# Kernel tuning notes

Measured on AMD Instinct MI355X. Metric: run time of the kernel, lower is better.

## Reference

```python
import math
import jax, jax.numpy as jnp
import numpy as np

D_MODEL = 1024
HEADS = 16
B, S = 4, 2048


def setup_inputs() -> dict:
    key = jax.random.key(0)
    ks = jax.random.split(key, 8)
    scale = 1.0 / math.sqrt(D_MODEL)
    return {
        "q": jax.random.normal(ks[0], (B, S, D_MODEL), dtype=jnp.float32),
        "k": jax.random.normal(ks[1], (B, S, D_MODEL), dtype=jnp.float32),
        "v": jax.random.normal(ks[2], (B, S, D_MODEL), dtype=jnp.float32),
        "mask": jax.random.randint(ks[3], (B, S), 0, 2).astype(jnp.bool_),
        "alibi_mask": jax.random.normal(ks[4], (1, HEADS, S, S), dtype=jnp.float32),
        "Wq": jax.random.normal(ks[5], (D_MODEL, D_MODEL), dtype=jnp.float32) * scale,
        "Wk": jax.random.normal(ks[6], (D_MODEL, D_MODEL), dtype=jnp.float32) * scale,
        "Wv": jax.random.normal(ks[7], (D_MODEL, D_MODEL), dtype=jnp.float32) * scale,
    }


def _split_heads(x):
    b, s, d = x.shape
    return x.reshape(b, s, HEADS, d // HEADS).transpose(0, 2, 1, 3)  # [B,H,S,hd]


def reference(q, k, v, mask, alibi_mask, Wq, Wk, Wv):
    # QKV projections (Linear, no bias)
    qh = _split_heads(q @ Wq)
    kh = _split_heads(k @ Wk)
    vh = _split_heads(v @ Wv)
    depth = qh.shape[-1]
    # naive full attention matrix [B,H,Sq,Sk]
    w = jnp.einsum("bhqd,bhkd->bhqk", qh, kh) / math.sqrt(depth)
    # mask: [B,Sk] -> [B,1,1,Sk], True = masked
    w = jnp.where(mask[:, None, None, :], -jnp.inf, w)
    w = w + alibi_mask
    a = jax.nn.softmax(w, axis=-1)  # dropout p=0 -> identity
    out = jnp.einsum("bhqk,bhkd->bhqd", a, vh)
    # combine heads -> [B,S,D]
    out = out.transpose(0, 2, 1, 3).reshape(q.shape[0], q.shape[1], -1)
    return (out, a)
```

## Files before the change

### kernel.cpp

```cpp
#include <hip/hip_runtime.h>
#include <hip/hip_bf16.h>
#include <math.h>

constexpr int B  = 4;
constexpr int S  = 2048;
constexpr int D  = 1024;
constexpr int H  = 16;
constexpr int HD = 64;
constexpr float LOG2E  = 1.4426950408889634f;
constexpr float SCALE2 = 0.125f * LOG2E;

using f32x4 = __attribute__((ext_vector_type(4))) float;
using s16x8 = __attribute__((ext_vector_type(8))) short;
using u16x8 = __attribute__((ext_vector_type(8))) unsigned short;
using u16x4 = __attribute__((ext_vector_type(4))) unsigned short;

__device__ __forceinline__ unsigned short f2bf(float f) {
    union { float f; unsigned u; } x; x.f = f;
    unsigned r = x.u + 0x7fffu + ((x.u >> 16) & 1u);
    return (unsigned short)(r >> 16);
}
__device__ __forceinline__ unsigned short f2bf_fast(float f) {
    union { float f; unsigned u; } x; x.f = f;
    return (unsigned short)((x.u + 0x8000u) >> 16);
}
__device__ __forceinline__ float bf2f(unsigned short h) {
    union { unsigned u; float f; } x; x.u = ((unsigned)h) << 16;
    return x.f;
}
__device__ __forceinline__ float fexp2(float x) {
#if __has_builtin(__builtin_amdgcn_exp2f)
    return __builtin_amdgcn_exp2f(x);
#else
    return __expf(x * 0.6931471805599453f);
#endif
}

#define MFMA_BF16(Af, Bf, Cf) __builtin_amdgcn_mfma_f32_16x16x32_bf16(Af, Bf, Cf, 0, 0, 0)

__global__ __launch_bounds__(256) void k_wt3(const float* __restrict__ Wq,
                                             const float* __restrict__ Wk,
                                             const float* __restrict__ Wv,
                                             unsigned short* __restrict__ wqt,
                                             unsigned short* __restrict__ wkt,
                                             unsigned short* __restrict__ wvt) {
    const float* W = blockIdx.z == 0 ? Wq : (blockIdx.z == 1 ? Wk : Wv);
    unsigned short* Wt = blockIdx.z == 0 ? wqt : (blockIdx.z == 1 ? wkt : wvt);
    __shared__ unsigned short T[64][68];
    const int k0 = blockIdx.x * 64, n0 = blockIdx.y * 64;
    const int t = threadIdx.x;
    {
        const int kr = t >> 4, nc4 = (t & 15) * 4;
        for (int rr = 0; rr < 4; ++rr) {
            const int kk = kr + rr * 16;
            f32x4 wv = *reinterpret_cast<const f32x4*>(&W[(size_t)(k0 + kk) * D + n0 + nc4]);
#pragma unroll
            for (int j = 0; j < 4; ++j) T[nc4 + j][kk] = f2bf(wv[j]);
        }
    }
    __syncthreads();
    {
        const int nr = t >> 4, kc4 = (t & 15) * 4;
        for (int rr = 0; rr < 4; ++rr) {
            const int nn = nr + rr * 16;
            u16x4 o;
#pragma unroll
            for (int j = 0; j < 4; ++j) o[j] = T[nn][kc4 + j];
            *reinterpret_cast<u16x4*>(&Wt[(size_t)(n0 + nn) * D + k0 + kc4]) = o;
        }
    }
}

__global__ __launch_bounds__(256) void k_proj2(const float* __restrict__ Xq,
                                               const float* __restrict__ Xk,
                                               const unsigned short* __restrict__ wqt,
                                               const unsigned short* __restrict__ wkt,
                                               unsigned short* __restrict__ qh,
                                               unsigned short* __restrict__ kh) {
    const float* X = blockIdx.z == 0 ? Xq : Xk;
    const unsigned short* Wt = blockIdx.z == 0 ? wqt : wkt;
    unsigned short* Y = blockIdx.z == 0 ? qh : kh;

    __shared__ alignas(16) unsigned short As[128][72];
    __shared__ alignas(16) unsigned short Bs[128][72];
    const int bm = blockIdx.y * 128, bn = blockIdx.x * 128;
    const int t = threadIdx.x, w = t >> 6, l = t & 63;
    const int wr = w >> 1, wc = w & 1;
    const int lr = l & 15, lg = l >> 4;
    f32x4 acc[4][4] = {};

    for (int k0 = 0; k0 < D; k0 += 64) {
        {
            const int c4 = (t & 15) * 4;
            int row = t >> 4;
            for (int rr = 0; rr < 8; ++rr, row += 16) {
                f32x4 xv = *reinterpret_cast<const f32x4*>(&X[(size_t)(bm + row) * D + k0 + c4]);
                u16x4 hv;
#pragma unroll
                for (int j = 0; j < 4; ++j) hv[j] = f2bf(xv[j]);
                *reinterpret_cast<u16x4*>(&As[row][c4]) = hv;
            }
        }
        for (int i = 0; i < 4; ++i) {
            const int idx = t + i * 256;
            const int row = idx >> 3, c8 = (idx & 7) * 8;
            *reinterpret_cast<u16x8*>(&Bs[row][c8]) =
                *reinterpret_cast<const u16x8*>(&Wt[(size_t)(bn + row) * D + k0 + c8]);
        }
        __syncthreads();
#pragma unroll
        for (int kk = 0; kk < 2; ++kk) {
            s16x8 af[4], bf[4];
#pragma unroll
            for (int f = 0; f < 4; ++f) {
                af[f] = *reinterpret_cast<const s16x8*>(&As[wr * 64 + f * 16 + lr][kk * 32 + lg * 8]);
                bf[f] = *reinterpret_cast<const s16x8*>(&Bs[wc * 64 + f * 16 + lr][kk * 32 + lg * 8]);
            }
#pragma unroll
            for (int fm = 0; fm < 4; ++fm)
#pragma unroll
                for (int fn = 0; fn < 4; ++fn)
                    acc[fm][fn] = MFMA_BF16(af[fm], bf[fn], acc[fm][fn]);
        }
        __syncthreads();
    }
#pragma unroll
    for (int fm = 0; fm < 4; ++fm)
#pragma unroll
        for (int fn = 0; fn < 4; ++fn)
#pragma unroll
            for (int r = 0; r < 4; ++r) {
                const int m = bm + wr * 64 + fm * 16 + lg * 4 + r;
                const int n = bn + wc * 64 + fn * 16 + lr;
                const int b = m >> 11, s = m & (S - 1);
                const int h = n >> 6, e = n & 63;
                Y[(((size_t)(b * H + h) * S) + s) * HD + e] = f2bf(acc[fm][fn][r]);
            }
}

__global__ __launch_bounds__(256) void k_projv_mfma(const float* __restrict__ X,
                                                    const unsigned short* __restrict__ Wt,
                                                    unsigned short* __restrict__ VT) {
    __shared__ alignas(16) unsigned short SM[2][128][72];
    unsigned short (*As)[72] = SM[0];
    unsigned short (*Bs)[72] = SM[1];
    const int bm = blockIdx.y * 128, bn = blockIdx.x * 128;
    const int t = threadIdx.x, w = t >> 6, l = t & 63;
    const int wr = w >> 1, wc = w & 1;
    const int lr = l & 15, lg = l >> 4;
    f32x4 acc[4][4] = {};

    for (int k0 = 0; k0 < D; k0 += 64) {
        {
            const int c4 = (t & 15) * 4;
            int row = t >> 4;
            for (int rr = 0; rr < 8; ++rr, row += 16) {
                f32x4 xv = *reinterpret_cast<const f32x4*>(&X[(size_t)(bm + row) * D + k0 + c4]);
                u16x4 hv;
#pragma unroll
                for (int j = 0; j < 4; ++j) hv[j] = f2bf(xv[j]);
                *reinterpret_cast<u16x4*>(&As[row][c4]) = hv;
            }
        }
        for (int i = 0; i < 4; ++i) {
            const int idx = t + i * 256;
            const int row = idx >> 3, c8 = (idx & 7) * 8;
            *reinterpret_cast<u16x8*>(&Bs[row][c8]) =
                *reinterpret_cast<const u16x8*>(&Wt[(size_t)(bn + row) * D + k0 + c8]);
        }
        __syncthreads();
#pragma unroll
        for (int kk = 0; kk < 2; ++kk) {
            s16x8 af[4], bf[4];
#pragma unroll
            for (int f = 0; f < 4; ++f) {
                af[f] = *reinterpret_cast<const s16x8*>(&As[wr * 64 + f * 16 + lr][kk * 32 + lg * 8]);
                bf[f] = *reinterpret_cast<const s16x8*>(&Bs[wc * 64 + f * 16 + lr][kk * 32 + lg * 8]);
            }
#pragma unroll
            for (int fm = 0; fm < 4; ++fm)
#pragma unroll
                for (int fn = 0; fn < 4; ++fn)
                    acc[fm][fn] = MFMA_BF16(af[fm], bf[fn], acc[fm][fn]);
        }
        __syncthreads();
    }
    unsigned short (*T)[144] = reinterpret_cast<unsigned short(*)[144]>(&SM[0][0][0]);
#pragma unroll
    for (int fm = 0; fm < 4; ++fm)
#pragma unroll
        for (int fn = 0; fn < 4; ++fn)
#pragma unroll
            for (int r = 0; r < 4; ++r)
                T[wc * 64 + fn * 16 + lr][wr * 64 + fm * 16 + lg * 4 + r] = f2bf(acc[fm][fn][r]);
    __syncthreads();
    const int b = bm >> 11, s0 = bm & (S - 1);
    for (int it = 0; it < 8; ++it) {
        const int idx = t + it * 256;
        const int row = idx >> 4, c8 = (idx & 15) * 8;
        const int h = (bn + row) >> 6, e = (bn + row) & 63;
        *reinterpret_cast<u16x8*>(&VT[((size_t)(b * H + h) * HD + e) * S + s0 + c8]) =
            *reinterpret_cast<const u16x8*>(&T[row][c8]);
    }
}

__global__ __launch_bounds__(256) void k_abf16(const float* __restrict__ A,
                                               unsigned short* __restrict__ O) {
    const size_t N = (size_t)H * S * S;
    const size_t stride = (size_t)gridDim.x * 256 * 8;
    for (size_t i = ((size_t)blockIdx.x * 256 + threadIdx.x) * 8; i < N; i += stride) {
        f32x4 a0 = *reinterpret_cast<const f32x4*>(&A[i]);
        f32x4 a1 = *reinterpret_cast<const f32x4*>(&A[i + 4]);
        u16x8 o;
#pragma unroll
        for (int j = 0; j < 4; ++j) {
            o[j]     = f2bf(a0[j] * LOG2E);
            o[4 + j] = f2bf(a1[j] * LOG2E);
        }
        *reinterpret_cast<u16x8*>(&O[i]) = o;
    }
}

template <bool ABF16>
__global__ __launch_bounds__(512, 4) void k_sumexp(
    const unsigned short* __restrict__ QH, const unsigned short* __restrict__ KH,
    const float* __restrict__ ALIBI, const unsigned short* __restrict__ ABF,
    const int* __restrict__ MASK, float* __restrict__ INVL) {
    __shared__ alignas(16) unsigned short Ks[64][72];
    __shared__ alignas(16) unsigned short ALs[128][72];

    const int bid = blockIdx.x;
    const int wg = (bid & 7) * 128 + (bid >> 3);
    const int bh = wg >> 4, b = bh >> 4, h = bh & 15;
    const int q0 = (wg & 15) * 128;
    const int t = threadIdx.x, w = t >> 6, ln = t & 63;
    const int lr = ln & 15, lg = ln >> 4;
    const unsigned short NEGBIG = f2bf(-1e30f);
    const size_t hoff = (size_t)h * S * S;

    const unsigned short* Kb = KH + (size_t)bh * S * HD;

    s16x8 qf[2];
#pragma unroll
    for (int kk = 0; kk < 2; ++kk)
        qf[kk] = *reinterpret_cast<const s16x8*>(
            &QH[((size_t)bh * S + q0 + w * 16 + lr) * HD + kk * 32 + lg * 8]);

    float psum = 0.f;

    for (int k0 = 0; k0 < S; k0 += 64) {
        {
            const int row = t >> 3, c8 = (t & 7) * 8;
            *reinterpret_cast<u16x8*>(&Ks[row][c8]) =
                *reinterpret_cast<const u16x8*>(&Kb[(size_t)(k0 + row) * HD + c8]);
        }
#pragma unroll
        for (int i = 0; i < 2; ++i) {
            const int idx = t + i * 512, row = idx >> 3, c8 = (idx & 7) * 8;
            int4 m0 = *reinterpret_cast<const int4*>(&MASK[b * S + k0 + c8]);
            int4 m1 = *reinterpret_cast<const int4*>(&MASK[b * S + k0 + c8 + 4]);
            u16x8 av;
            if constexpr (ABF16) {
                av = *reinterpret_cast<const u16x8*>(&ABF[hoff + (size_t)(q0 + row) * S + k0 + c8]);
            } else {
                f32x4 a0 = *reinterpret_cast<const f32x4*>(&ALIBI[hoff + (size_t)(q0 + row) * S + k0 + c8]);
                f32x4 a1 = *reinterpret_cast<const f32x4*>(&ALIBI[hoff + (size_t)(q0 + row) * S + k0 + c8 + 4]);
#pragma unroll
                for (int j = 0; j < 4; ++j) {
                    av[j] = f2bf(a0[j] * LOG2E);
                    av[4 + j] = f2bf(a1[j] * LOG2E);
                }
            }
            u16x8 sv;
            sv[0] = m0.x ? NEGBIG : av[0];
            sv[1] = m0.y ? NEGBIG : av[1];
            sv[2] = m0.z ? NEGBIG : av[2];
            sv[3] = m0.w ? NEGBIG : av[3];
            sv[4] = m1.x ? NEGBIG : av[4];
            sv[5] = m1.y ? NEGBIG : av[5];
            sv[6] = m1.z ? NEGBIG : av[6];
            sv[7] = m1.w ? NEGBIG : av[7];
            *reinterpret_cast<u16x8*>(&ALs[row][c8]) = sv;
        }
        __syncthreads();

        f32x4 acc[4] = {};
#pragma unroll
        for (int kk = 0; kk < 2; ++kk)
#pragma unroll
            for (int fn = 0; fn < 4; ++fn) {
                s16x8 kf = *reinterpret_cast<const s16x8*>(&Ks[fn * 16 + lr][kk * 32 + lg * 8]);
                acc[fn] = MFMA_BF16(kf, qf[kk], acc[fn]);
            }
#pragma unroll
        for (int fn = 0; fn < 4; ++fn) {
            u16x4 alv = *reinterpret_cast<const u16x4*>(&ALs[w * 16 + lr][fn * 16 + lg * 4]);
            f32x4 al;
#pragma unroll
            for (int j = 0; j < 4; ++j) al[j] = bf2f(alv[j]);
            f32x4 sv = acc[fn] * SCALE2 + al;
            psum += fexp2(sv[0]) + fexp2(sv[1]) + fexp2(sv[2]) + fexp2(sv[3]);
        }
        __syncthreads();
    }

    psum += __shfl_xor(psum, 16, 64);
    psum += __shfl_xor(psum, 32, 64);
    if (lg == 0)
        INVL[(size_t)bh * S + q0 + w * 16 + lr] = 1.0f / psum;
}

template <bool ABF16>
__global__ __launch_bounds__(512, 4) void k_attn(
    const unsigned short* __restrict__ QH, const unsigned short* __restrict__ KH,
    const unsigned short* __restrict__ VT, const float* __restrict__ ALIBI,
    const unsigned short* __restrict__ ABF, const int* __restrict__ MASK,
    const float* __restrict__ INVL, float* __restrict__ Aout,
    float* __restrict__ OUT) {
    __shared__ alignas(16) unsigned short Ks[64][72];
    __shared__ alignas(16) unsigned short Vs[64][72];
    __shared__ alignas(16) unsigned short ALs[128][72];

    const int bid = blockIdx.x;
    const int wg = (bid & 7) * 128 + (bid >> 3);
    const int bh = wg >> 4, b = bh >> 4, h = bh & 15;
    const int q0 = (wg & 15) * 128;
    const int t = threadIdx.x, w = t >> 6, ln = t & 63;
    const int lr = ln & 15, lg = ln >> 4;
    const unsigned short NEGBIG = f2bf(-1e30f);
    const size_t hoff = (size_t)h * S * S;

    const unsigned short* Kb = KH + (size_t)bh * S * HD;
    const unsigned short* Vb = VT + (size_t)bh * HD * S;

    s16x8 qf[2];
#pragma unroll
    for (int kk = 0; kk < 2; ++kk)
        qf[kk] = *reinterpret_cast<const s16x8*>(
            &QH[((size_t)bh * S + q0 + w * 16 + lr) * HD + kk * 32 + lg * 8]);

    const float invl = INVL[(size_t)bh * S + q0 + w * 16 + lr];
    float* arow = Aout + ((size_t)bh * S + q0 + w * 16 + lr) * S;

    f32x4 oacc[4] = {};

    for (int k0 = 0; k0 < S; k0 += 64) {
        {
            const int row = t >> 3, c8 = (t & 7) * 8;
            *reinterpret_cast<u16x8*>(&Ks[row][c8]) =
                *reinterpret_cast<const u16x8*>(&Kb[(size_t)(k0 + row) * HD + c8]);
            *reinterpret_cast<u16x8*>(&Vs[row][c8]) =
                *reinterpret_cast<const u16x8*>(&Vb[(size_t)row * S + k0 + c8]);
        }
#pragma unroll
        for (int i = 0; i < 2; ++i) {
            const int idx = t + i * 512, row = idx >> 3, c8 = (idx & 7) * 8;
            int4 m0 = *reinterpret_cast<const int4*>(&MASK[b * S + k0 + c8]);
            int4 m1 = *reinterpret_cast<const int4*>(&MASK[b * S + k0 + c8 + 4]);
            u16x8 av;
            if constexpr (ABF16) {
                av = *reinterpret_cast<const u16x8*>(&ABF[hoff + (size_t)(q0 + row) * S + k0 + c8]);
            } else {
                f32x4 a0 = *reinterpret_cast<const f32x4*>(&ALIBI[hoff + (size_t)(q0 + row) * S + k0 + c8]);
                f32x4 a1 = *reinterpret_cast<const f32x4*>(&ALIBI[hoff + (size_t)(q0 + row) * S + k0 + c8 + 4]);
#pragma unroll
                for (int j = 0; j < 4; ++j) {
                    av[j] = f2bf(a0[j] * LOG2E);
                    av[4 + j] = f2bf(a1[j] * LOG2E);
                }
            }
            u16x8 sv;
            sv[0] = m0.x ? NEGBIG : av[0];
            sv[1] = m0.y ? NEGBIG : av[1];
            sv[2] = m0.z ? NEGBIG : av[2];
            sv[3] = m0.w ? NEGBIG : av[3];
            sv[4] = m1.x ? NEGBIG : av[4];
            sv[5] = m1.y ? NEGBIG : av[5];
            sv[6] = m1.z ? NEGBIG : av[6];
            sv[7] = m1.w ? NEGBIG : av[7];
            *reinterpret_cast<u16x8*>(&ALs[row][c8]) = sv;
        }
        __syncthreads();

        f32x4 acc[4] = {};
#pragma unroll
        for (int kk = 0; kk < 2; ++kk)
#pragma unroll
            for (int fn = 0; fn < 4; ++fn) {
                s16x8 kf = *reinterpret_cast<const s16x8*>(&Ks[fn * 16 + lr][kk * 32 + lg * 8]);
                acc[fn] = MFMA_BF16(kf, qf[kk], acc[fn]);
            }

#pragma unroll
        for (int fn = 0; fn < 4; ++fn) {
            u16x4 alv = *reinterpret_cast<const u16x4*>(&ALs[w * 16 + lr][fn * 16 + lg * 4]);
            f32x4 al;
#pragma unroll
            for (int j = 0; j < 4; ++j) al[j] = bf2f(alv[j]);
            f32x4 sv = acc[fn] * SCALE2 + al;
            f32x4 p;
#pragma unroll
            for (int j = 0; j < 4; ++j) p[j] = fexp2(sv[j]);
            p *= invl;
            __builtin_nontemporal_store(
                p, reinterpret_cast<f32x4*>(arow + k0 + fn * 16 + lg * 4));
            u16x4 pb;
#pragma unroll
            for (int j = 0; j < 4; ++j) pb[j] = f2bf_fast(p[j]);
            *reinterpret_cast<u16x4*>(&ALs[w * 16 + lr][fn * 16 + lg * 4]) = pb;
        }

#pragma unroll
        for (int c = 0; c < 2; ++c) {
            s16x8 pa = *reinterpret_cast<const s16x8*>(&ALs[w * 16 + lr][c * 32 + lg * 8]);
#pragma unroll
            for (int fn = 0; fn < 4; ++fn) {
                s16x8 vf = *reinterpret_cast<const s16x8*>(&Vs[fn * 16 + lr][c * 32 + lg * 8]);
                oacc[fn] = MFMA_BF16(pa, vf, oacc[fn]);
            }
        }
        __syncthreads();
    }

#pragma unroll
    for (int fn = 0; fn < 4; ++fn)
#pragma unroll
        for (int r = 0; r < 4; ++r)
            OUT[(size_t)(b * S + q0 + w * 16 + lg * 4 + r) * D + h * HD + fn * 16 + lr] =
                oacc[fn][r];
}

extern "C" void kernel_launch(void* const* d_in, const int* in_sizes, int n_in,
                              void* d_out, int out_size, void* d_ws, size_t ws_size,
                              hipStream_t stream) {
    const float* q     = (const float*)d_in[0];
    const float* k     = (const float*)d_in[1];
    const float* v     = (const float*)d_in[2];
    const int*   mask  = (const int*)d_in[3];
    const float* alibi = (const float*)d_in[4];
    const float* Wq    = (const float*)d_in[5];
    const float* Wk    = (const float*)d_in[6];
    const float* Wv    = (const float*)d_in[7];

    float* out = (float*)d_out;
    float* a   = out + (size_t)B * S * D;

    const size_t NH = (size_t)B * H * S * HD;
    unsigned short* qh  = (unsigned short*)d_ws;
    unsigned short* kh  = qh + NH;
    unsigned short* vT  = kh + NH;
    unsigned short* wqt = vT + NH;
    unsigned short* wkt = wqt + (size_t)D * D;
    unsigned short* wvt = wkt + (size_t)D * D;
    float*          invl = (float*)(wvt + (size_t)D * D);
    unsigned short* abf  = (unsigned short*)(invl + (size_t)B * H * S);

    const size_t need_bf16 =
        ((size_t)(abf - qh) + (size_t)H * S * S) * sizeof(unsigned short);
    const bool use_abf16 = ws_size >= need_bf16;

    const dim3 blk(256);

    k_wt3<<<dim3(D / 64, D / 64, 3), blk, 0, stream>>>(Wq, Wk, Wv, wqt, wkt, wvt);

    if (use_abf16)
        k_abf16<<<dim3(8192), blk, 0, stream>>>(alibi, abf);

    k_proj2<<<dim3(D / 128, (B * S) / 128, 2), blk, 0, stream>>>(q, k, wqt, wkt, qh, kh);
    k_projv_mfma<<<dim3(D / 128, (B * S) / 128), blk, 0, stream>>>(v, wvt, vT);

    if (use_abf16) {
        k_sumexp<true><<<dim3(1024), dim3(512), 0, stream>>>(
            qh, kh, alibi, abf, mask, invl);
        k_attn<true><<<dim3(1024), dim3(512), 0, stream>>>(
            qh, kh, vT, alibi, abf, mask, invl, a, out);
    } else {
        k_sumexp<false><<<dim3(1024), dim3(512), 0, stream>>>(
            qh, kh, alibi, abf, mask, invl);
        k_attn<false><<<dim3(1024), dim3(512), 0, stream>>>(
            qh, kh, vT, alibi, abf, mask, invl, a, out);
    }
}
```

Before: 665.3 us.

## Read fp32 alibi and mask directly in registers, drop bf16 pre-pass, double-buffer K/V

Removes the separate kernel that converted the alibi bias to bf16 and the shared-memory staging of bias+mask. Each lane now loads its fp32 alibi and mask values straight from global memory and folds them in with an fma. K/V tiles are double-buffered in shared memory so the next tile loads while the current one computes, and one barrier per iteration is removed. This cuts total alibi traffic and a launch, but relies on uncoalesced per-row global loads in the inner loop.

```diff
diff --git a/kernel.cpp b/kernel.cpp
--- a/kernel.cpp
+++ b/kernel.cpp
@@ -23,10 +23,6 @@
 __device__ __forceinline__ unsigned short f2bf_fast(float f) {
     union { float f; unsigned u; } x; x.f = f;
     return (unsigned short)((x.u + 0x8000u) >> 16);
-}
-__device__ __forceinline__ float bf2f(unsigned short h) {
-    union { unsigned u; float f; } x; x.u = ((unsigned)h) << 16;
-    return x.f;
 }
 __device__ __forceinline__ float fexp2(float x) {
 #if __has_builtin(__builtin_amdgcn_exp2f)
@@ -204,30 +200,11 @@
     }
 }
 
-__global__ __launch_bounds__(256) void k_abf16(const float* __restrict__ A,
-                                               unsigned short* __restrict__ O) {
-    const size_t N = (size_t)H * S * S;
-    const size_t stride = (size_t)gridDim.x * 256 * 8;
-    for (size_t i = ((size_t)blockIdx.x * 256 + threadIdx.x) * 8; i < N; i += stride) {
-        f32x4 a0 = *reinterpret_cast<const f32x4*>(&A[i]);
-        f32x4 a1 = *reinterpret_cast<const f32x4*>(&A[i + 4]);
-        u16x8 o;
-#pragma unroll
-        for (int j = 0; j < 4; ++j) {
-            o[j]     = f2bf(a0[j] * LOG2E);
-            o[4 + j] = f2bf(a1[j] * LOG2E);
-        }
-        *reinterpret_cast<u16x8*>(&O[i]) = o;
-    }
-}
-
-template <bool ABF16>
 __global__ __launch_bounds__(512, 4) void k_sumexp(
     const unsigned short* __restrict__ QH, const unsigned short* __restrict__ KH,
-    const float* __restrict__ ALIBI, const unsigned short* __restrict__ ABF,
-    const int* __restrict__ MASK, float* __restrict__ INVL) {
-    __shared__ alignas(16) unsigned short Ks[64][72];
-    __shared__ alignas(16) unsigned short ALs[128][72];
+    const float* __restrict__ ALIBI, const int* __restrict__ MASK,
+    float* __restrict__ INVL) {
+    __shared__ alignas(16) unsigned short Ks[2][64][72];
 
     const int bid = blockIdx.x;
     const int wg = (bid & 7) * 128 + (bid >> 3);
@@ -235,10 +212,10 @@
     const int q0 = (wg & 15) * 128;
     const int t = threadIdx.x, w = t >> 6, ln = t & 63;
     const int lr = ln & 15, lg = ln >> 4;
-    const unsigned short NEGBIG = f2bf(-1e30f);
-    const size_t hoff = (size_t)h * S * S;
 
     const unsigned short* Kb = KH + (size_t)bh * S * HD;
+    const float* alrow = ALIBI + ((size_t)h * S + q0 + w * 16 + lr) * S;
+    const int* mrow = MASK + b * S;
 
     s16x8 qf[2];
 #pragma unroll
@@ -246,62 +223,41 @@
         qf[kk] = *reinterpret_cast<const s16x8*>(
             &QH[((size_t)bh * S + q0 + w * 16 + lr) * HD + kk * 32 + lg * 8]);
 
+    auto stage_k = [&](int buf, int k0) {
+        const int row = t >> 3, c8 = (t & 7) * 8;
+        *reinterpret_cast<u16x8*>(&Ks[buf][row][c8]) =
+            *reinterpret_cast<const u16x8*>(&Kb[(size_t)(k0 + row) * HD + c8]);
+    };
+
     float psum = 0.f;
-
-    for (int k0 = 0; k0 < S; k0 += 64) {
-        {
-            const int row = t >> 3, c8 = (t & 7) * 8;
-            *reinterpret_cast<u16x8*>(&Ks[row][c8]) =
-                *reinterpret_cast<const u16x8*>(&Kb[(size_t)(k0 + row) * HD + c8]);
-        }
-#pragma unroll
-        for (int i = 0; i < 2; ++i) {
-            const int idx = t + i * 512, row = idx >> 3, c8 = (idx & 7) * 8;
-            int4 m0 = *reinterpret_cast<const int4*>(&MASK[b * S + k0 + c8]);
-            int4 m1 = *reinterpret_cast<const int4*>(&MASK[b * S + k0 + c8 + 4]);
-            u16x8 av;
-            if constexpr (ABF16) {
-                av = *reinterpret_cast<const u16x8*>(&ABF[hoff + (size_t)(q0 + row) * S + k0 + c8]);
-            } else {
-                f32x4 a0 = *reinterpret_cast<const f32x4*>(&ALIBI[hoff + (size_t)(q0 + row) * S + k0 + c8]);
-                f32x4 a1 = *reinterpret_cast<const f32x4*>(&ALIBI[hoff + (size_t)(q0 + row) * S + k0 + c8 + 4]);
-#pragma unroll
-                for (int j = 0; j < 4; ++j) {
-                    av[j] = f2bf(a0[j] * LOG2E);
-                    av[4 + j] = f2bf(a1[j] * LOG2E);
-                }
-            }
-            u16x8 sv;
-            sv[0] = m0.x ? NEGBIG : av[0];
-            sv[1] = m0.y ? NEGBIG : av[1];
-            sv[2] = m0.z ? NEGBIG : av[2];
-            sv[3] = m0.w ? NEGBIG : av[3];
-            sv[4] = m1.x ? NEGBIG : av[4];
-            sv[5] = m1.y ? NEGBIG : av[5];
-            sv[6] = m1.z ? NEGBIG : av[6];
-            sv[7] = m1.w ? NEGBIG : av[7];
-            *reinterpret_cast<u16x8*>(&ALs[row][c8]) = sv;
-        }
-        __syncthreads();
+    stage_k(0, 0);
+
+    for (int t16 = 0; t16 < 32; ++t16) {
+        const int cur = t16 & 1;
+        const int k0 = t16 * 64;
+        __syncthreads();
+        if (t16 < 31) stage_k(cur ^ 1, k0 + 64);
 
         f32x4 acc[4] = {};
 #pragma unroll
         for (int kk = 0; kk < 2; ++kk)
 #pragma unroll
             for (int fn = 0; fn < 4; ++fn) {
-                s16x8 kf = *reinterpret_cast<const s16x8*>(&Ks[fn * 16 + lr][kk * 32 + lg * 8]);
+                s16x8 kf = *reinterpret_cast<const s16x8*>(&Ks[cur][fn * 16 + lr][kk * 32 + lg * 8]);
                 acc[fn] = MFMA_BF16(kf, qf[kk], acc[fn]);
             }
 #pragma unroll
         for (int fn = 0; fn < 4; ++fn) {
-            u16x4 alv = *reinterpret_cast<const u16x4*>(&ALs[w * 16 + lr][fn * 16 + lg * 4]);
-            f32x4 al;
-#pragma unroll
-            for (int j = 0; j < 4; ++j) al[j] = bf2f(alv[j]);
-            f32x4 sv = acc[fn] * SCALE2 + al;
+            const int kc = k0 + fn * 16 + lg * 4;
+            f32x4 al = *reinterpret_cast<const f32x4*>(&alrow[kc]);
+            int4 mv = *reinterpret_cast<const int4*>(&mrow[kc]);
+            f32x4 sv;
+            sv[0] = mv.x ? -1e30f : fmaf(al[0], LOG2E, acc[fn][0] * SCALE2);
+            sv[1] = mv.y ? -1e30f : fmaf(al[1], LOG2E, acc[fn][1] * SCALE2);
+            sv[2] = mv.z ? -1e30f : fmaf(al[2], LOG2E, acc[fn][2] * SCALE2);
+            sv[3] = mv.w ? -1e30f : fmaf(al[3], LOG2E, acc[fn][3] * SCALE2);
             psum += fexp2(sv[0]) + fexp2(sv[1]) + fexp2(sv[2]) + fexp2(sv[3]);
         }
-        __syncthreads();
     }
 
     psum += __shfl_xor(psum, 16, 64);
@@ -310,16 +266,14 @@
         INVL[(size_t)bh * S + q0 + w * 16 + lr] = 1.0f / psum;
 }
 
-template <bool ABF16>
 __global__ __launch_bounds__(512, 4) void k_attn(
     const unsigned short* __restrict__ QH, const unsigned short* __restrict__ KH,
     const unsigned short* __restrict__ VT, const float* __restrict__ ALIBI,
-    const unsigned short* __restrict__ ABF, const int* __restrict__ MASK,
-    const float* __restrict__ INVL, float* __restrict__ Aout,
-    float* __restrict__ OUT) {
-    __shared__ alignas(16) unsigned short Ks[64][72];
-    __shared__ alignas(16) unsigned short Vs[64][72];
-    __shared__ alignas(16) unsigned short ALs[128][72];
+    const int* __restrict__ MASK, const float* __restrict__ INVL,
+    float* __restrict__ Aout, float* __restrict__ OUT) {
+    __shared__ alignas(16) unsigned short Ks[2][64][72];
+    __shared__ alignas(16) unsigned short Vs[2][64][72];
+    __shared__ alignas(16) unsigned short Ps[128][72];
 
     const int bid = blockIdx.x;
     const int wg = (bid & 7) * 128 + (bid >> 3);
@@ -327,11 +281,11 @@
     const int q0 = (wg & 15) * 128;
     const int t = threadIdx.x, w = t >> 6, ln = t & 63;
     const int lr = ln & 15, lg = ln >> 4;
-    const unsigned short NEGBIG = f2bf(-1e30f);
-    const size_t hoff = (size_t)h * S * S;
 
     const unsigned short* Kb = KH + (size_t)bh * S * HD;
     const unsigned short* Vb = VT + (size_t)bh * HD * S;
+    const float* alrow = ALIBI + ((size_t)h * S + q0 + w * 16 + lr) * S;
+    const int* mrow = MASK + b * S;
 
     s16x8 qf[2];
 #pragma unroll
@@ -342,84 +296,63 @@
     const float invl = INVL[(size_t)bh * S + q0 + w * 16 + lr];
     float* arow = Aout + ((size_t)bh * S + q0 + w * 16 + lr) * S;
 
+    auto stage_kv = [&](int buf, int k0) {
+        const int row = t >> 3, c8 = (t & 7) * 8;
+        *reinterpret_cast<u16x8*>(&Ks[buf][row][c8]) =
+            *reinterpret_cast<const u16x8*>(&Kb[(size_t)(k0 + row) * HD + c8]);
+        *reinterpret_cast<u16x8*>(&Vs[buf][row][c8]) =
+            *reinterpret_cast<const u16x8*>(&Vb[(size_t)row * S + k0 + c8]);
+    };
+
     f32x4 oacc[4] = {};
-
-    for (int k0 = 0; k0 < S; k0 += 64) {
-        {
-            const int row = t >> 3, c8 = (t & 7) * 8;
-            *reinterpret_cast<u16x8*>(&Ks[row][c8]) =
-                *reinterpret_cast<const u16x8*>(&Kb[(size_t)(k0 + row) * HD + c8]);
-            *reinterpret_cast<u16x8*>(&Vs[row][c8]) =
-                *reinterpret_cast<const u16x8*>(&Vb[(size_t)row * S + k0 + c8]);
-        }
-#pragma unroll
-        for (int i = 0; i < 2; ++i) {
-            const int idx = t + i * 512, row = idx >> 3, c8 = (idx & 7) * 8;
-            int4 m0 = *reinterpret_cast<const int4*>(&MASK[b * S + k0 + c8]);
-            int4 m1 = *reinterpret_cast<const int4*>(&MASK[b * S + k0 + c8 + 4]);
-            u16x8 av;
-            if constexpr (ABF16) {
-                av = *reinterpret_cast<const u16x8*>(&ABF[hoff + (size_t)(q0 + row) * S + k0 + c8]);
-            } else {
-                f32x4 a0 = *reinterpret_cast<const f32x4*>(&ALIBI[hoff + (size_t)(q0 + row) * S + k0 + c8]);
-                f32x4 a1 = *reinterpret_cast<const f32x4*>(&ALIBI[hoff + (size_t)(q0 + row) * S + k0 + c8 + 4]);
-#pragma unroll
-                for (int j = 0; j < 4; ++j) {
-                    av[j] = f2bf(a0[j] * LOG2E);
-                    av[4 + j] = f2bf(a1[j] * LOG2E);
-                }
-            }
-            u16x8 sv;
-            sv[0] = m0.x ? NEGBIG : av[0];
-            sv[1] = m0.y ? NEGBIG : av[1];
-            sv[2] = m0.z ? NEGBIG : av[2];
-            sv[3] = m0.w ? NEGBIG : av[3];
-            sv[4] = m1.x ? NEGBIG : av[4];
-            sv[5] = m1.y ? NEGBIG : av[5];
-            sv[6] = m1.z ? NEGBIG : av[6];
-            sv[7] = m1.w ? NEGBIG : av[7];
-            *reinterpret_cast<u16x8*>(&ALs[row][c8]) = sv;
-        }
-        __syncthreads();
+    stage_kv(0, 0);
+
+    for (int t16 = 0; t16 < 32; ++t16) {
+        const int cur = t16 & 1;
+        const int k0 = t16 * 64;
+        __syncthreads();
+        if (t16 < 31) stage_kv(cur ^ 1, k0 + 64);
 
         f32x4 acc[4] = {};
 #pragma unroll
         for (int kk = 0; kk < 2; ++kk)
 #pragma unroll
             for (int fn = 0; fn < 4; ++fn) {
-                s16x8 kf = *reinterpret_cast<const s16x8*>(&Ks[fn * 16 + lr][kk * 32 + lg * 8]);
+                s16x8 kf = *reinterpret_cast<const s16x8*>(&Ks[cur][fn * 16 + lr][kk * 32 + lg * 8]);
                 acc[fn] = MFMA_BF16(kf, qf[kk], acc[fn]);
             }
 
 #pragma unroll
         for (int fn = 0; fn < 4; ++fn) {
-            u16x4 alv = *reinterpret_cast<const u16x4*>(&ALs[w * 16 + lr][fn * 16 + lg * 4]);
-            f32x4 al;
-#pragma unroll
-            for (int j = 0; j < 4; ++j) al[j] = bf2f(alv[j]);
-            f32x4 sv = acc[fn] * SCALE2 + al;
+            const int kc = k0 + fn * 16 + lg * 4;
+            f32x4 al = *reinterpret_cast<const f32x4*>(&alrow[kc]);
+            int4 mv = *reinterpret_cast<const int4*>(&mrow[kc]);
+            f32x4 sv;
+            sv[0] = mv.x ? -1e30f : fmaf(al[0], LOG2E, acc[fn][0] * SCALE2);
+            sv[1] = mv.y ? -1e30f : fmaf(al[1], LOG2E, acc[fn][1] * SCALE2);
+            sv[2] = mv.z ? -1e30f : fmaf(al[2], LOG2E, acc[fn][2] * SCALE2);
+            sv[3] = mv.w ? -1e30f : fmaf(al[3], LOG2E, acc[fn][3] * SCALE2);
             f32x4 p;
 #pragma unroll
             for (int j = 0; j < 4; ++j) p[j] = fexp2(sv[j]);
             p *= invl;
             __builtin_nontemporal_store(
-                p, reinterpret_cast<f32x4*>(arow + k0 + fn * 16 + lg * 4));
+                p, reinterpret_cast<f32x4*>(arow + kc));
             u16x4 pb;
 #pragma unroll
             for (int j = 0; j < 4; ++j) pb[j] = f2bf_fast(p[j]);
-            *reinterpret_cast<u16x4*>(&ALs[w * 16 + lr][fn * 16 + lg * 4]) = pb;
+            *reinterpret_cast<u16x4*>(&Ps[w * 16 + lr][fn * 16 + lg * 4]) = pb;
         }
 
 #pragma unroll
         for (int c = 0; c < 2; ++c) {
-            s16x8 pa = *reinterpret_cast<const s16x8*>(&ALs[w * 16 + lr][c * 32 + lg * 8]);
+            s16x8 pa = *reinterpret_cast<const s16x8*>(&Ps[w * 16 + lr][c * 32 + lg * 8]);
 #pragma unroll
             for (int fn = 0; fn < 4; ++fn) {
-                s16x8 vf = *reinterpret_cast<const s16x8*>(&Vs[fn * 16 + lr][c * 32 + lg * 8]);
+                s16x8 vf = *reinterpret_cast<const s16x8*>(&Vs[cur][fn * 16 + lr][c * 32 + lg * 8]);
                 oacc[fn] = MFMA_BF16(pa, vf, oacc[fn]);
             }
         }
-        __syncthreads();
     }
 
 #pragma unroll
@@ -453,31 +386,14 @@
     unsigned short* wkt = wqt + (size_t)D * D;
     unsigned short* wvt = wkt + (size_t)D * D;
     float*          invl = (float*)(wvt + (size_t)D * D);
-    unsigned short* abf  = (unsigned short*)(invl + (size_t)B * H * S);
-
-    const size_t need_bf16 =
-        ((size_t)(abf - qh) + (size_t)H * S * S) * sizeof(unsigned short);
-    const bool use_abf16 = ws_size >= need_bf16;
 
     const dim3 blk(256);
 
     k_wt3<<<dim3(D / 64, D / 64, 3), blk, 0, stream>>>(Wq, Wk, Wv, wqt, wkt, wvt);
-
-    if (use_abf16)
-        k_abf16<<<dim3(8192), blk, 0, stream>>>(alibi, abf);
 
     k_proj2<<<dim3(D / 128, (B * S) / 128, 2), blk, 0, stream>>>(q, k, wqt, wkt, qh, kh);
     k_projv_mfma<<<dim3(D / 128, (B * S) / 128), blk, 0, stream>>>(v, wvt, vT);
 
-    if (use_abf16) {
-        k_sumexp<true><<<dim3(1024), dim3(512), 0, stream>>>(
-            qh, kh, alibi, abf, mask, invl);
-        k_attn<true><<<dim3(1024), dim3(512), 0, stream>>>(
-            qh, kh, vT, alibi, abf, mask, invl, a, out);
-    } else {
-        k_sumexp<false><<<dim3(1024), dim3(512), 0, stream>>>(
-            qh, kh, alibi, abf, mask, invl);
-        k_attn<false><<<dim3(1024), dim3(512), 0, stream>>>(
-            qh, kh, vT, alibi, abf, mask, invl, a, out);
-    }
-}
+    k_sumexp<<<dim3(1024), dim3(512), 0, stream>>>(qh, kh, alibi, mask, invl);
+    k_attn<<<dim3(1024), dim3(512), 0, stream>>>(qh, kh, vT, alibi, mask, invl, a, out);
+}
```

Result: slower. 756.4 us (+13.7%).

## Double-buffer K/V tiles and make alibi staging wave-private to drop a barrier

Applied to the files above, without the earlier changes.

Both attention kernels now double-buffer the K (and V) tiles in shared memory. Each wave loads only its own 16 rows of the alibi/mask tile, so the alibi tile can be restaged for the next step without a block barrier, leaving one __syncthreads per iteration instead of two. In k_attn, probabilities go to a separate Ps buffer so the alibi prefetch does not overwrite them. This hides global load latency behind MFMA and exp work, at the cost of more shared memory per block, which may lower occupancy under the 512x4 launch bounds.

```diff
diff --git a/kernel.cpp b/kernel.cpp
--- a/kernel.cpp
+++ b/kernel.cpp
@@ -226,7 +226,7 @@
     const unsigned short* __restrict__ QH, const unsigned short* __restrict__ KH,
     const float* __restrict__ ALIBI, const unsigned short* __restrict__ ABF,
     const int* __restrict__ MASK, float* __restrict__ INVL) {
-    __shared__ alignas(16) unsigned short Ks[64][72];
+    __shared__ alignas(16) unsigned short Ks[2][64][72];
     __shared__ alignas(16) unsigned short ALs[128][72];
 
     const int bid = blockIdx.x;
@@ -246,25 +246,26 @@
         qf[kk] = *reinterpret_cast<const s16x8*>(
             &QH[((size_t)bh * S + q0 + w * 16 + lr) * HD + kk * 32 + lg * 8]);
 
-    float psum = 0.f;
-
-    for (int k0 = 0; k0 < S; k0 += 64) {
-        {
-            const int row = t >> 3, c8 = (t & 7) * 8;
-            *reinterpret_cast<u16x8*>(&Ks[row][c8]) =
-                *reinterpret_cast<const u16x8*>(&Kb[(size_t)(k0 + row) * HD + c8]);
-        }
+    auto stage_k = [&](int buf, int k0) {
+        const int row = t >> 3, c8 = (t & 7) * 8;
+        *reinterpret_cast<u16x8*>(&Ks[buf][row][c8]) =
+            *reinterpret_cast<const u16x8*>(&Kb[(size_t)(k0 + row) * HD + c8]);
+    };
+    auto stage_al = [&](int k0) {
 #pragma unroll
         for (int i = 0; i < 2; ++i) {
-            const int idx = t + i * 512, row = idx >> 3, c8 = (idx & 7) * 8;
+            const int rowl = w * 16 + (ln >> 3) + i * 8;
+            const int c8 = (ln & 7) * 8;
             int4 m0 = *reinterpret_cast<const int4*>(&MASK[b * S + k0 + c8]);
             int4 m1 = *reinterpret_cast<const int4*>(&MASK[b * S + k0 + c8 + 4]);
             u16x8 av;
             if constexpr (ABF16) {
-                av = *reinterpret_cast<const u16x8*>(&ABF[hoff + (size_t)(q0 + row) * S + k0 + c8]);
+                av = *reinterpret_cast<const u16x8*>(
+                    &ABF[hoff + (size_t)(q0 + rowl) * S + k0 + c8]);
             } else {
-                f32x4 a0 = *reinterpret_cast<const f32x4*>(&ALIBI[hoff + (size_t)(q0 + row) * S + k0 + c8]);
-                f32x4 a1 = *reinterpret_cast<const f32x4*>(&ALIBI[hoff + (size_t)(q0 + row) * S + k0 + c8 + 4]);
+                const size_t goff = hoff + (size_t)(q0 + rowl) * S + k0 + c8;
+                f32x4 a0 = *reinterpret_cast<const f32x4*>(&ALIBI[goff]);
+                f32x4 a1 = *reinterpret_cast<const f32x4*>(&ALIBI[goff + 4]);
 #pragma unroll
                 for (int j = 0; j < 4; ++j) {
                     av[j] = f2bf(a0[j] * LOG2E);
@@ -280,16 +281,26 @@
             sv[5] = m1.y ? NEGBIG : av[5];
             sv[6] = m1.z ? NEGBIG : av[6];
             sv[7] = m1.w ? NEGBIG : av[7];
-            *reinterpret_cast<u16x8*>(&ALs[row][c8]) = sv;
-        }
+            *reinterpret_cast<u16x8*>(&ALs[rowl][c8]) = sv;
+        }
+    };
+
+    float psum = 0.f;
+    stage_k(0, 0);
+    stage_al(0);
+
+    for (int t16 = 0; t16 < 32; ++t16) {
+        const int cur = t16 & 1;
+        const int k0 = t16 * 64;
         __syncthreads();
+        if (t16 < 31) stage_k(cur ^ 1, k0 + 64);
 
         f32x4 acc[4] = {};
 #pragma unroll
         for (int kk = 0; kk < 2; ++kk)
 #pragma unroll
             for (int fn = 0; fn < 4; ++fn) {
-                s16x8 kf = *reinterpret_cast<const s16x8*>(&Ks[fn * 16 + lr][kk * 32 + lg * 8]);
+                s16x8 kf = *reinterpret_cast<const s16x8*>(&Ks[cur][fn * 16 + lr][kk * 32 + lg * 8]);
                 acc[fn] = MFMA_BF16(kf, qf[kk], acc[fn]);
             }
 #pragma unroll
@@ -301,7 +312,7 @@
             f32x4 sv = acc[fn] * SCALE2 + al;
             psum += fexp2(sv[0]) + fexp2(sv[1]) + fexp2(sv[2]) + fexp2(sv[3]);
         }
-        __syncthreads();
+        if (t16 < 31) stage_al(k0 + 64);
     }
 
     psum += __shfl_xor(psum, 16, 64);
@@ -317,9 +328,10 @@
     const unsigned short* __restrict__ ABF, const int* __restrict__ MASK,
     const float* __restrict__ INVL, float* __restrict__ Aout,
     float* __restrict__ OUT) {
-    __shared__ alignas(16) unsigned short Ks[64][72];
-    __shared__ alignas(16) unsigned short Vs[64][72];
+    __shared__ alignas(16) unsigned short Ks[2][64][72];
+    __shared__ alignas(16) unsigned short Vs[2][64][72];
     __shared__ alignas(16) unsigned short ALs[128][72];
+    __shared__ alignas(16) unsigned short Ps[128][72];
 
     const int bid = blockIdx.x;
     const int wg = (bid & 7) * 128 + (bid >> 3);
@@ -342,27 +354,28 @@
     const float invl = INVL[(size_t)bh * S + q0 + w * 16 + lr];
     float* arow = Aout + ((size_t)bh * S + q0 + w * 16 + lr) * S;
 
-    f32x4 oacc[4] = {};
-
-    for (int k0 = 0; k0 < S; k0 += 64) {
-        {
-            const int row = t >> 3, c8 = (t & 7) * 8;
-            *reinterpret_cast<u16x8*>(&Ks[row][c8]) =
-                *reinterpret_cast<const u16x8*>(&Kb[(size_t)(k0 + row) * HD + c8]);
-            *reinterpret_cast<u16x8*>(&Vs[row][c8]) =
-                *reinterpret_cast<const u16x8*>(&Vb[(size_t)row * S + k0 + c8]);
-        }
+    auto stage_kv = [&](int buf, int k0) {
+        const int row = t >> 3, c8 = (t & 7) * 8;
+        *reinterpret_cast<u16x8*>(&Ks[buf][row][c8]) =
+            *reinterpret_cast<const u16x8*>(&Kb[(size_t)(k0 + row) * HD + c8]);
+        *reinterpret_cast<u16x8*>(&Vs[buf][row][c8]) =
+            *reinterpret_cast<const u16x8*>(&Vb[(size_t)row * S + k0 + c8]);
+    };
+    auto stage_al = [&](int k0) {
 #pragma unroll
         for (int i = 0; i < 2; ++i) {
-            const int idx = t + i * 512, row = idx >> 3, c8 = (idx & 7) * 8;
+            const int rowl = w * 16 + (ln >> 3) + i * 8;
+            const int c8 = (ln & 7) * 8;
             int4 m0 = *reinterpret_cast<const int4*>(&MASK[b * S + k0 + c8]);
             int4 m1 = *reinterpret_cast<const int4*>(&MASK[b * S + k0 + c8 + 4]);
             u16x8 av;
             if constexpr (ABF16) {
-                av = *reinterpret_cast<const u16x8*>(&ABF[hoff + (size_t)(q0 + row) * S + k0 + c8]);
+                av = *reinterpret_cast<const u16x8*>(
+                    &ABF[hoff + (size_t)(q0 + rowl) * S + k0 + c8]);
             } else {
-                f32x4 a0 = *reinterpret_cast<const f32x4*>(&ALIBI[hoff + (size_t)(q0 + row) * S + k0 + c8]);
-                f32x4 a1 = *reinterpret_cast<const f32x4*>(&ALIBI[hoff + (size_t)(q0 + row) * S + k0 + c8 + 4]);
+                const size_t goff = hoff + (size_t)(q0 + rowl) * S + k0 + c8;
+                f32x4 a0 = *reinterpret_cast<const f32x4*>(&ALIBI[goff]);
+                f32x4 a1 = *reinterpret_cast<const f32x4*>(&ALIBI[goff + 4]);
 #pragma unroll
                 for (int j = 0; j < 4; ++j) {
                     av[j] = f2bf(a0[j] * LOG2E);
@@ -378,16 +391,26 @@
             sv[5] = m1.y ? NEGBIG : av[5];
             sv[6] = m1.z ? NEGBIG : av[6];
             sv[7] = m1.w ? NEGBIG : av[7];
-            *reinterpret_cast<u16x8*>(&ALs[row][c8]) = sv;
-        }
+            *reinterpret_cast<u16x8*>(&ALs[rowl][c8]) = sv;
+        }
+    };
+
+    f32x4 oacc[4] = {};
+    stage_kv(0, 0);
+    stage_al(0);
+
+    for (int t16 = 0; t16 < 32; ++t16) {
+        const int cur = t16 & 1;
+        const int k0 = t16 * 64;
         __syncthreads();
+        if (t16 < 31) stage_kv(cur ^ 1, k0 + 64);
 
         f32x4 acc[4] = {};
 #pragma unroll
         for (int kk = 0; kk < 2; ++kk)
 #pragma unroll
             for (int fn = 0; fn < 4; ++fn) {
-                s16x8 kf = *reinterpret_cast<const s16x8*>(&Ks[fn * 16 + lr][kk * 32 + lg * 8]);
+                s16x8 kf = *reinterpret_cast<const s16x8*>(&Ks[cur][fn * 16 + lr][kk * 32 + lg * 8]);
                 acc[fn] = MFMA_BF16(kf, qf[kk], acc[fn]);
             }
 
@@ -407,19 +430,20 @@
             u16x4 pb;
 #pragma unroll
             for (int j = 0; j < 4; ++j) pb[j] = f2bf_fast(p[j]);
-            *reinterpret_cast<u16x4*>(&ALs[w * 16 + lr][fn * 16 + lg * 4]) = pb;
-        }
+            *reinterpret_cast<u16x4*>(&Ps[w * 16 + lr][fn * 16 + lg * 4]) = pb;
+        }
+
+        if (t16 < 31) stage_al(k0 + 64);
 
 #pragma unroll
         for (int c = 0; c < 2; ++c) {
-            s16x8 pa = *reinterpret_cast<const s16x8*>(&ALs[w * 16 + lr][c * 32 + lg * 8]);
+            s16x8 pa = *reinterpret_cast<const s16x8*>(&Ps[w * 16 + lr][c * 32 + lg * 8]);
 #pragma unroll
             for (int fn = 0; fn < 4; ++fn) {
-                s16x8 vf = *reinterpret_cast<const s16x8*>(&Vs[fn * 16 + lr][c * 32 + lg * 8]);
+                s16x8 vf = *reinterpret_cast<const s16x8*>(&Vs[cur][fn * 16 + lr][c * 32 + lg * 8]);
                 oacc[fn] = MFMA_BF16(pa, vf, oacc[fn]);
             }
         }
-        __syncthreads();
     }
 
 #pragma unroll
```

Result: slower. 686.2 us (median of 2 runs) (+3.1%).
